# Kernel tuning notes

Measured on AMD Instinct MI355X. Metric: run time of the kernel, lower is better.

The kernel has to match this reference:

```python
import jax, jax.numpy as jnp
import numpy as np

BLOCK_SIZES = [256] * 8            # sum = N_CTX = 2048
B, H, D = 2, 16, 64
N_CTX = sum(BLOCK_SIZES)
SPARSITY_PATTERN = 'block_causal'  # row_starts = 0, row_ends = end of own block


def _build_masks(block_sizes, pattern):
    cs = np.cumsum([0] + list(block_sizes))
    row_ends = np.concatenate([np.full(bs, cs[i + 1], dtype=np.int32)
                               for i, bs in enumerate(block_sizes)])
    if pattern == 'block_diagonal':
        row_starts = np.concatenate([np.full(bs, cs[i], dtype=np.int32)
                                     for i, bs in enumerate(block_sizes)])
    elif pattern == 'block_causal':
        row_starts = np.zeros_like(row_ends)
    else:
        raise ValueError(pattern)
    return jnp.asarray(row_starts), jnp.asarray(row_ends)


def setup_inputs() -> dict:
    key = jax.random.key(0)
    kq, kk, kv = jax.random.split(key, 3)
    q = jax.random.normal(kq, (B, H, N_CTX, D), dtype=jnp.float32)
    k = jax.random.normal(kk, (B, H, N_CTX, D), dtype=jnp.float32)
    v = jax.random.normal(kv, (B, H, N_CTX, D), dtype=jnp.float32)
    row_starts, row_ends = _build_masks(BLOCK_SIZES, SPARSITY_PATTERN)
    sm_scale = jnp.float32(1.0 / np.sqrt(D))
    return {"q": q, "k": k, "v": v, "sm_scale": sm_scale,
            "row_starts": row_starts, "row_ends": row_ends}


def reference(q, k, v, sm_scale, row_starts, row_ends):
    # q,k,v: [B,H,N,D]; per query row i, attend to kv cols in [row_starts[i], row_ends[i])
    n = q.shape[2]
    cols = jnp.arange(n, dtype=jnp.int32)
    allowed = (cols[None, :] >= row_starts[:, None]) & (cols[None, :] < row_ends[:, None])  # [N,N]
    scores = jnp.einsum('bhqd,bhkd->bhqk', q, k) * sm_scale
    neg = jnp.finfo(scores.dtype).min
    scores = jnp.where(allowed[None, None], scores, neg)
    p = jax.nn.softmax(scores, axis=-1)
    return jnp.einsum('bhqk,bhkd->bhqd', p, v)
```

## Files before the change

kernel.cpp:

```cpp
#include <hip/hip_runtime.h>


typedef short bf16x8 __attribute__((ext_vector_type(8)));
typedef float f32x4  __attribute__((ext_vector_type(4)));
typedef unsigned short u16;
typedef u16 u16x8 __attribute__((ext_vector_type(8)));

#define MFMA(A,B,C) __builtin_amdgcn_mfma_f32_16x16x32_bf16((A),(B),(C),0,0,0)

__device__ __forceinline__ u16 f2bf_rne(float f) {
    union { float f; unsigned u; } c; c.f = f;
    unsigned r = c.u + 0x7FFFu + ((c.u >> 16) & 1u);
    return (u16)(r >> 16);
}
__device__ __forceinline__ u16 f2bf_fast(float f) {
    union { float f; unsigned u; } c; c.f = f;
    return (u16)((c.u + 0x8000u) >> 16);
}

__device__ __forceinline__ void gload_lds16(const void* g, void* lds) {
    __builtin_amdgcn_global_load_lds(
        (const __attribute__((address_space(1))) unsigned int*)g,
        (__attribute__((address_space(3))) unsigned int*)lds, 16, 0, 0);
}

__global__ __launch_bounds__(256)
void prep_kernel(const float* __restrict__ K, const float* __restrict__ V,
                 u16* __restrict__ blob)
{
    int bt = blockIdx.x;
    int tid = threadIdx.x;
    const size_t gbase = (size_t)bt * 4096;
    u16* bb = blob + (size_t)bt * 8192;
    __shared__ __align__(16) u16 lt[4096];
    {
        int key = tid >> 2, c2 = (tid & 3) << 1;
        int rotb = (key & 3) + 4 * ((key >> 3) & 1);
        const float* kp = K + gbase + key * 64 + c2 * 8;
        float4 x0 = *(const float4*)kp,       x1 = *(const float4*)(kp + 4);
        float4 x2 = *(const float4*)(kp + 8), x3 = *(const float4*)(kp + 12);
        u16x8 a, b;
        a[0]=f2bf_rne(x0.x); a[1]=f2bf_rne(x0.y); a[2]=f2bf_rne(x0.z); a[3]=f2bf_rne(x0.w);
        a[4]=f2bf_rne(x1.x); a[5]=f2bf_rne(x1.y); a[6]=f2bf_rne(x1.z); a[7]=f2bf_rne(x1.w);
        b[0]=f2bf_rne(x2.x); b[1]=f2bf_rne(x2.y); b[2]=f2bf_rne(x2.z); b[3]=f2bf_rne(x2.w);
        b[4]=f2bf_rne(x3.x); b[5]=f2bf_rne(x3.y); b[6]=f2bf_rne(x3.z); b[7]=f2bf_rne(x3.w);
        *(u16x8*)&bb[key * 64 + (((c2    ) + rotb) & 7) * 8] = a;
        *(u16x8*)&bb[key * 64 + (((c2 + 1) + rotb) & 7) * 8] = b;
    }
    {
        int wv = tid >> 6, ln = tid & 63;
        const float* vp = V + gbase + ln * 64 + wv * 16;
        float4 y0 = *(const float4*)vp,       y1 = *(const float4*)(vp + 4);
        float4 y2 = *(const float4*)(vp + 8), y3 = *(const float4*)(vp + 12);
        float yy[16] = { y0.x,y0.y,y0.z,y0.w, y1.x,y1.y,y1.z,y1.w,
                         y2.x,y2.y,y2.z,y2.w, y3.x,y3.y,y3.z,y3.w };
        int kc = ln >> 3, kw = ln & 7;
        #pragma unroll
        for (int j = 0; j < 16; ++j) {
            int d = wv * 16 + j;
            lt[d * 64 + ((kc + (j & 7)) & 7) * 8 + kw] = f2bf_rne(yy[j]);
        }
    }
    __syncthreads();
    {
        int o = tid * 16;
        *(u16x8*)&bb[4096 + o]     = *(const u16x8*)&lt[o];
        *(u16x8*)&bb[4096 + o + 8] = *(const u16x8*)&lt[o + 8];
    }
}

__global__ __launch_bounds__(256, 4)
void bsattn_main(const float* __restrict__ Q, const float* __restrict__ SC,
                 const int* __restrict__ RS, const int* __restrict__ RE,
                 const u16* __restrict__ blob, float* __restrict__ O)
{
    constexpr int N = 2048, D = 64;
    int wg = blockIdx.x;
    int bh = wg & 31;
    int i0 = wg >> 5, kk = i0 & 7, rr = i0 >> 3;
    int qt = (rr == 0) ? ((kk < 4) ? 28 + kk : 20 + kk)
           : (rr == 1) ? ((kk < 4) ? 20 + kk : 12 + kk)
           : (rr == 2) ? (8 + kk) : kk;
    int q0 = qt << 6;

    int tid = threadIdx.x, wid = tid >> 6, lane = tid & 63;
    int n = lane & 15, g = lane >> 4;

    __shared__ __align__(16) u16 lsm[16384];
    __shared__ int sbi[16];

    int myrow = q0 + wid * 16 + n;
    int rs_l = RS[myrow], re_l = RE[myrow];
    int w_rs_min = rs_l, w_rs_max = rs_l, w_re_min = re_l, w_re_max = re_l;
    #pragma unroll
    for (int o = 1; o < 16; o <<= 1) {
        w_rs_min = min(w_rs_min, __shfl_xor(w_rs_min, o));
        w_rs_max = max(w_rs_max, __shfl_xor(w_rs_max, o));
        w_re_min = min(w_re_min, __shfl_xor(w_re_min, o));
        w_re_max = max(w_re_max, __shfl_xor(w_re_max, o));
    }
    if (lane == 0) { sbi[wid * 2] = w_rs_min; sbi[wid * 2 + 1] = w_re_max; }

    float sscale = SC[0] * 1.44269504088896340736f;

    bf16x8 qf0, qf1;
    {
        const float* qp = Q + ((size_t)bh * N + myrow) * D + g * 8;
        float4 a0 = *(const float4*)qp,        a1 = *(const float4*)(qp + 4);
        float4 b0 = *(const float4*)(qp + 32), b1 = *(const float4*)(qp + 36);
        qf0[0]=f2bf_rne(a0.x*sscale); qf0[1]=f2bf_rne(a0.y*sscale);
        qf0[2]=f2bf_rne(a0.z*sscale); qf0[3]=f2bf_rne(a0.w*sscale);
        qf0[4]=f2bf_rne(a1.x*sscale); qf0[5]=f2bf_rne(a1.y*sscale);
        qf0[6]=f2bf_rne(a1.z*sscale); qf0[7]=f2bf_rne(a1.w*sscale);
        qf1[0]=f2bf_rne(b0.x*sscale); qf1[1]=f2bf_rne(b0.y*sscale);
        qf1[2]=f2bf_rne(b0.z*sscale); qf1[3]=f2bf_rne(b0.w*sscale);
        qf1[4]=f2bf_rne(b1.x*sscale); qf1[5]=f2bf_rne(b1.y*sscale);
        qf1[6]=f2bf_rne(b1.z*sscale); qf1[7]=f2bf_rne(b1.w*sscale);
    }

    __syncthreads();
    int kst  = min(min(sbi[0], sbi[2]), min(sbi[4], sbi[6])) & ~63;
    int kend = max(max(sbi[1], sbi[3]), max(sbi[5], sbi[7]));
    int t0 = kst >> 6;
    int w  = (kend - kst + 63) >> 6;

    int rA   = ((n >> 2) << 3) + (n & 3);
    int phk  = (n & 3) + 4 * ((n >> 2) & 1);
    int osA0 = rA * 64 + ((g + phk) & 7) * 8;
    int osA1 = rA * 64 + ((g + 4 + phk) & 7) * 8;
    int ov0  = 4096 + n * 64 + ((    g + (n & 7)) & 7) * 8;
    int ov1  = 4096 + n * 64 + ((4 + g + (n & 7)) & 7) * 8;

    f32x4 acc[4], accl = {0.f, 0.f, 0.f, 0.f};
    #pragma unroll
    for (int c = 0; c < 4; ++c) acc[c] = (f32x4){0.f, 0.f, 0.f, 0.f};
    bf16x8 ones;
    #pragma unroll
    for (int j = 0; j < 8; ++j) ones[j] = (short)0x3F80;

    auto stage = [&](int i) {
        if (i < w) {
            const u16* src = blob + (size_t)(bh * 32 + t0 + i) * 8192;
            u16* dst = &lsm[(i & 1) << 13];
            int wb = wid * 2048;
            #pragma unroll
            for (int c = 0; c < 4; ++c)
                gload_lds16(src + wb + c * 512 + lane * 8, dst + wb + c * 512);
        }
    };

    auto proc = [&](int kb, const u16* ls) {
        float sc[16];
        #pragma unroll
        for (int h = 0; h < 2; ++h) {
            int hb = h * 2048;
            f32x4 t0v = {0.f,0.f,0.f,0.f}, t1v = t0v;
            t0v = MFMA(*(const bf16x8*)&ls[hb + osA0],       qf0, t0v);
            t0v = MFMA(*(const bf16x8*)&ls[hb + osA1],       qf1, t0v);
            t1v = MFMA(*(const bf16x8*)&ls[hb + osA0 + 256], qf0, t1v);
            t1v = MFMA(*(const bf16x8*)&ls[hb + osA1 + 256], qf1, t1v);
            #pragma unroll
            for (int r = 0; r < 4; ++r) { sc[h*8 + r] = t0v[r]; sc[h*8 + 4 + r] = t1v[r]; }
        }
        if (kb < w_rs_max || kb + 64 > w_re_min) {
            #pragma unroll
            for (int h = 0; h < 2; ++h)
                #pragma unroll
                for (int j = 0; j < 8; ++j) {
                    int key = kb + h * 32 + g * 8 + j;
                    if (key < rs_l || key >= re_l) sc[h*8 + j] = -1e30f;
                }
        }
        bf16x8 pf0, pf1;
        #pragma unroll
        for (int j = 0; j < 8; ++j) { float p = __builtin_amdgcn_exp2f(sc[j]);     pf0[j] = (short)f2bf_fast(p); }
        #pragma unroll
        for (int j = 0; j < 8; ++j) { float p = __builtin_amdgcn_exp2f(sc[8 + j]); pf1[j] = (short)f2bf_fast(p); }
        #pragma unroll
        for (int h = 0; h < 2; ++h) {
            const bf16x8& pf = h ? pf1 : pf0;
            int ov = h ? ov1 : ov0;
            acc[0] = MFMA(pf, *(const bf16x8*)&ls[ov       ], acc[0]);
            acc[1] = MFMA(pf, *(const bf16x8*)&ls[ov + 1024], acc[1]);
            acc[2] = MFMA(pf, *(const bf16x8*)&ls[ov + 2048], acc[2]);
            acc[3] = MFMA(pf, *(const bf16x8*)&ls[ov + 3072], acc[3]);
            accl   = MFMA(pf, ones, accl);
        }
    };

    stage(0);
    for (int i = 0; i < w; ++i) {
        __syncthreads();
        stage(i + 1);
        proc(kst + (i << 6), &lsm[(i & 1) << 13]);
    }

    int rb = g << 2;
    int orow = q0 + wid * 16 + rb;
    float* ob = O + ((size_t)bh * N + orow) * D + n;
    #pragma unroll
    for (int r = 0; r < 4; ++r) {
        float li = 1.0f / accl[r];
        float* rp = ob + (size_t)r * D;
        rp[0]  = acc[0][r] * li;
        rp[16] = acc[1][r] * li;
        rp[32] = acc[2][r] * li;
        rp[48] = acc[3][r] * li;
    }
}

extern "C" void kernel_launch(void* const* d_in, const int* in_sizes, int n_in,
                              void* d_out, int out_size, void* d_ws, size_t ws_size,
                              hipStream_t stream) {
    const float* q  = (const float*)d_in[0];
    const float* k  = (const float*)d_in[1];
    const float* v  = (const float*)d_in[2];
    const float* sc = (const float*)d_in[3];
    const int* rs   = (const int*)d_in[4];
    const int* re   = (const int*)d_in[5];
    float* out      = (float*)d_out;
    u16* blob       = (u16*)d_ws;

    prep_kernel<<<dim3(1024), dim3(256), 0, stream>>>(k, v, blob);
    bsattn_main<<<dim3(1024), dim3(256), 0, stream>>>(q, sc, rs, re, blob, out);
}
```

Baseline: 131.4 us.

## Switch to single-wave 32x32x16 MFMA tiles with barrier-free double buffering

Rewrites the attention kernel so each workgroup is one 64-lane wave handling 32 query rows. It uses 32x32x16 bf16 MFMAs instead of 16x16x32, with new K/V LDS swizzles to match, set in the prep kernel. Workgroup barriers are replaced by vmcnt waits, and the wave prefetches two tiles ahead. Each wave now stages the full 16 KB K/V tile into LDS by itself, so global-to-LDS traffic grows per query row and occupancy depends on LDS per 64-thread block.

```diff
diff --git a/kernel.cpp b/kernel.cpp
--- a/kernel.cpp
+++ b/kernel.cpp
@@ -2,11 +2,11 @@
 
 
 typedef short bf16x8 __attribute__((ext_vector_type(8)));
-typedef float f32x4  __attribute__((ext_vector_type(4)));
+typedef float f32x16 __attribute__((ext_vector_type(16)));
 typedef unsigned short u16;
 typedef u16 u16x8 __attribute__((ext_vector_type(8)));
 
-#define MFMA(A,B,C) __builtin_amdgcn_mfma_f32_16x16x32_bf16((A),(B),(C),0,0,0)
+#define MFMA32(A,B,C) __builtin_amdgcn_mfma_f32_32x32x16_bf16((A),(B),(C),0,0,0)
 
 __device__ __forceinline__ u16 f2bf_rne(float f) {
     union { float f; unsigned u; } c; c.f = f;
@@ -17,7 +17,6 @@
     union { float f; unsigned u; } c; c.f = f;
     return (u16)((c.u + 0x8000u) >> 16);
 }
-
 __device__ __forceinline__ void gload_lds16(const void* g, void* lds) {
     __builtin_amdgcn_global_load_lds(
         (const __attribute__((address_space(1))) unsigned int*)g,
@@ -33,9 +32,11 @@
     const size_t gbase = (size_t)bt * 4096;
     u16* bb = blob + (size_t)bt * 8192;
     __shared__ __align__(16) u16 lt[4096];
-    {
-        int key = tid >> 2, c2 = (tid & 3) << 1;
-        int rotb = (key & 3) + 4 * ((key >> 3) & 1);
+
+    int key = tid >> 2;
+    int dg  = tid & 3;
+    {
+        int c2 = dg << 1;
         const float* kp = K + gbase + key * 64 + c2 * 8;
         float4 x0 = *(const float4*)kp,       x1 = *(const float4*)(kp + 4);
         float4 x2 = *(const float4*)(kp + 8), x3 = *(const float4*)(kp + 12);
@@ -44,21 +45,22 @@
         a[4]=f2bf_rne(x1.x); a[5]=f2bf_rne(x1.y); a[6]=f2bf_rne(x1.z); a[7]=f2bf_rne(x1.w);
         b[0]=f2bf_rne(x2.x); b[1]=f2bf_rne(x2.y); b[2]=f2bf_rne(x2.z); b[3]=f2bf_rne(x2.w);
         b[4]=f2bf_rne(x3.x); b[5]=f2bf_rne(x3.y); b[6]=f2bf_rne(x3.z); b[7]=f2bf_rne(x3.w);
-        *(u16x8*)&bb[key * 64 + (((c2    ) + rotb) & 7) * 8] = a;
-        *(u16x8*)&bb[key * 64 + (((c2 + 1) + rotb) & 7) * 8] = b;
-    }
-    {
-        int wv = tid >> 6, ln = tid & 63;
-        const float* vp = V + gbase + ln * 64 + wv * 16;
+        *(u16x8*)&bb[key * 64 + (((c2    ) + key) & 7) * 8] = a;
+        *(u16x8*)&bb[key * 64 + (((c2 + 1) + key) & 7) * 8] = b;
+    }
+    {
+        int sl = (key & 51) | ((key & 4) << 1) | ((key & 8) >> 1);
+        int sh = sl >> 3, sw = sl & 7;
+        const float* vp = V + gbase + key * 64 + dg * 16;
         float4 y0 = *(const float4*)vp,       y1 = *(const float4*)(vp + 4);
         float4 y2 = *(const float4*)(vp + 8), y3 = *(const float4*)(vp + 12);
         float yy[16] = { y0.x,y0.y,y0.z,y0.w, y1.x,y1.y,y1.z,y1.w,
                          y2.x,y2.y,y2.z,y2.w, y3.x,y3.y,y3.z,y3.w };
-        int kc = ln >> 3, kw = ln & 7;
         #pragma unroll
         for (int j = 0; j < 16; ++j) {
-            int d = wv * 16 + j;
-            lt[d * 64 + ((kc + (j & 7)) & 7) * 8 + kw] = f2bf_rne(yy[j]);
+            int d = dg * 16 + j;
+            int p = (sh + (j & 7) + 2 * dg) & 7;
+            lt[d * 64 + p * 8 + sw] = f2bf_rne(yy[j]);
         }
     }
     __syncthreads();
@@ -69,7 +71,7 @@
     }
 }
 
-__global__ __launch_bounds__(256, 4)
+__global__ __launch_bounds__(64)
 void bsattn_main(const float* __restrict__ Q, const float* __restrict__ SC,
                  const int* __restrict__ RS, const int* __restrict__ RE,
                  const u16* __restrict__ blob, float* __restrict__ O)
@@ -77,135 +79,122 @@
     constexpr int N = 2048, D = 64;
     int wg = blockIdx.x;
     int bh = wg & 31;
-    int i0 = wg >> 5, kk = i0 & 7, rr = i0 >> 3;
-    int qt = (rr == 0) ? ((kk < 4) ? 28 + kk : 20 + kk)
-           : (rr == 1) ? ((kk < 4) ? 20 + kk : 12 + kk)
-           : (rr == 2) ? (8 + kk) : kk;
-    int q0 = qt << 6;
-
-    int tid = threadIdx.x, wid = tid >> 6, lane = tid & 63;
-    int n = lane & 15, g = lane >> 4;
+    int qs = 63 - (wg >> 5);
+    int q0w = qs << 5;
+    int lane = threadIdx.x;
+    int n5 = lane & 31, h5 = lane >> 5;
 
     __shared__ __align__(16) u16 lsm[16384];
-    __shared__ int sbi[16];
-
-    int myrow = q0 + wid * 16 + n;
+
+    int myrow = q0w + n5;
     int rs_l = RS[myrow], re_l = RE[myrow];
     int w_rs_min = rs_l, w_rs_max = rs_l, w_re_min = re_l, w_re_max = re_l;
     #pragma unroll
-    for (int o = 1; o < 16; o <<= 1) {
+    for (int o = 1; o < 32; o <<= 1) {
         w_rs_min = min(w_rs_min, __shfl_xor(w_rs_min, o));
         w_rs_max = max(w_rs_max, __shfl_xor(w_rs_max, o));
         w_re_min = min(w_re_min, __shfl_xor(w_re_min, o));
         w_re_max = max(w_re_max, __shfl_xor(w_re_max, o));
     }
-    if (lane == 0) { sbi[wid * 2] = w_rs_min; sbi[wid * 2 + 1] = w_re_max; }
 
     float sscale = SC[0] * 1.44269504088896340736f;
 
-    bf16x8 qf0, qf1;
-    {
-        const float* qp = Q + ((size_t)bh * N + myrow) * D + g * 8;
-        float4 a0 = *(const float4*)qp,        a1 = *(const float4*)(qp + 4);
-        float4 b0 = *(const float4*)(qp + 32), b1 = *(const float4*)(qp + 36);
-        qf0[0]=f2bf_rne(a0.x*sscale); qf0[1]=f2bf_rne(a0.y*sscale);
-        qf0[2]=f2bf_rne(a0.z*sscale); qf0[3]=f2bf_rne(a0.w*sscale);
-        qf0[4]=f2bf_rne(a1.x*sscale); qf0[5]=f2bf_rne(a1.y*sscale);
-        qf0[6]=f2bf_rne(a1.z*sscale); qf0[7]=f2bf_rne(a1.w*sscale);
-        qf1[0]=f2bf_rne(b0.x*sscale); qf1[1]=f2bf_rne(b0.y*sscale);
-        qf1[2]=f2bf_rne(b0.z*sscale); qf1[3]=f2bf_rne(b0.w*sscale);
-        qf1[4]=f2bf_rne(b1.x*sscale); qf1[5]=f2bf_rne(b1.y*sscale);
-        qf1[6]=f2bf_rne(b1.z*sscale); qf1[7]=f2bf_rne(b1.w*sscale);
-    }
-
-    __syncthreads();
-    int kst  = min(min(sbi[0], sbi[2]), min(sbi[4], sbi[6])) & ~63;
-    int kend = max(max(sbi[1], sbi[3]), max(sbi[5], sbi[7]));
-    int t0 = kst >> 6;
-    int w  = (kend - kst + 63) >> 6;
-
-    int rA   = ((n >> 2) << 3) + (n & 3);
-    int phk  = (n & 3) + 4 * ((n >> 2) & 1);
-    int osA0 = rA * 64 + ((g + phk) & 7) * 8;
-    int osA1 = rA * 64 + ((g + 4 + phk) & 7) * 8;
-    int ov0  = 4096 + n * 64 + ((    g + (n & 7)) & 7) * 8;
-    int ov1  = 4096 + n * 64 + ((4 + g + (n & 7)) & 7) * 8;
-
-    f32x4 acc[4], accl = {0.f, 0.f, 0.f, 0.f};
-    #pragma unroll
-    for (int c = 0; c < 4; ++c) acc[c] = (f32x4){0.f, 0.f, 0.f, 0.f};
+    bf16x8 qf[4];
+    {
+        const float* qp = Q + ((size_t)bh * N + myrow) * D + h5 * 8;
+        #pragma unroll
+        for (int s = 0; s < 4; ++s) {
+            float4 x0 = *(const float4*)(qp + 16 * s);
+            float4 x1 = *(const float4*)(qp + 16 * s + 4);
+            qf[s][0] = f2bf_rne(x0.x * sscale); qf[s][1] = f2bf_rne(x0.y * sscale);
+            qf[s][2] = f2bf_rne(x0.z * sscale); qf[s][3] = f2bf_rne(x0.w * sscale);
+            qf[s][4] = f2bf_rne(x1.x * sscale); qf[s][5] = f2bf_rne(x1.y * sscale);
+            qf[s][6] = f2bf_rne(x1.z * sscale); qf[s][7] = f2bf_rne(x1.w * sscale);
+        }
+    }
+
+    int kst = w_rs_min & ~63;
+    int w   = (w_re_max - kst + 63) >> 6;
+
+    int rot = (h5 + (n5 & 7)) & 7;
+    int offK[2][4], offV[2][4];
+    #pragma unroll
+    for (int s = 0; s < 4; ++s) {
+        offK[0][s] = n5 * 64        + (((2*s + rot)) & 7) * 8;
+        offK[1][s] = (32 + n5) * 64 + (((2*s + rot)) & 7) * 8;
+        int v0t = 2 * ((n5 >> 4) & 3);
+        int v1t = 2 * ((2 + (n5 >> 4)) & 3);
+        offV[0][s] = 4096 + n5 * 64        + ((2*s + rot + v0t) & 7) * 8;
+        offV[1][s] = 4096 + (32 + n5) * 64 + ((2*s + rot + v1t) & 7) * 8;
+    }
+
+    f32x16 acc0, acc1, accl;
+    #pragma unroll
+    for (int r = 0; r < 16; ++r) { acc0[r] = 0.f; acc1[r] = 0.f; accl[r] = 0.f; }
     bf16x8 ones;
     #pragma unroll
     for (int j = 0; j < 8; ++j) ones[j] = (short)0x3F80;
 
     auto stage = [&](int i) {
         if (i < w) {
-            const u16* src = blob + (size_t)(bh * 32 + t0 + i) * 8192;
+            const u16* src = blob + ((size_t)(bh * 32) + (kst >> 6) + i) * 8192;
             u16* dst = &lsm[(i & 1) << 13];
-            int wb = wid * 2048;
             #pragma unroll
-            for (int c = 0; c < 4; ++c)
-                gload_lds16(src + wb + c * 512 + lane * 8, dst + wb + c * 512);
+            for (int cc = 0; cc < 16; ++cc)
+                gload_lds16(src + cc * 512 + lane * 8, dst + cc * 512);
         }
     };
 
     auto proc = [&](int kb, const u16* ls) {
-        float sc[16];
-        #pragma unroll
-        for (int h = 0; h < 2; ++h) {
-            int hb = h * 2048;
-            f32x4 t0v = {0.f,0.f,0.f,0.f}, t1v = t0v;
-            t0v = MFMA(*(const bf16x8*)&ls[hb + osA0],       qf0, t0v);
-            t0v = MFMA(*(const bf16x8*)&ls[hb + osA1],       qf1, t0v);
-            t1v = MFMA(*(const bf16x8*)&ls[hb + osA0 + 256], qf0, t1v);
-            t1v = MFMA(*(const bf16x8*)&ls[hb + osA1 + 256], qf1, t1v);
-            #pragma unroll
-            for (int r = 0; r < 4; ++r) { sc[h*8 + r] = t0v[r]; sc[h*8 + 4 + r] = t1v[r]; }
+        f32x16 c0, c1;
+        #pragma unroll
+        for (int r = 0; r < 16; ++r) { c0[r] = 0.f; c1[r] = 0.f; }
+        #pragma unroll
+        for (int s = 0; s < 4; ++s) {
+            c0 = MFMA32(*(const bf16x8*)&ls[offK[0][s]], qf[s], c0);
+            c1 = MFMA32(*(const bf16x8*)&ls[offK[1][s]], qf[s], c1);
         }
         if (kb < w_rs_max || kb + 64 > w_re_min) {
             #pragma unroll
-            for (int h = 0; h < 2; ++h)
-                #pragma unroll
-                for (int j = 0; j < 8; ++j) {
-                    int key = kb + h * 32 + g * 8 + j;
-                    if (key < rs_l || key >= re_l) sc[h*8 + j] = -1e30f;
-                }
-        }
-        bf16x8 pf0, pf1;
-        #pragma unroll
-        for (int j = 0; j < 8; ++j) { float p = __builtin_amdgcn_exp2f(sc[j]);     pf0[j] = (short)f2bf_fast(p); }
-        #pragma unroll
-        for (int j = 0; j < 8; ++j) { float p = __builtin_amdgcn_exp2f(sc[8 + j]); pf1[j] = (short)f2bf_fast(p); }
-        #pragma unroll
-        for (int h = 0; h < 2; ++h) {
-            const bf16x8& pf = h ? pf1 : pf0;
-            int ov = h ? ov1 : ov0;
-            acc[0] = MFMA(pf, *(const bf16x8*)&ls[ov       ], acc[0]);
-            acc[1] = MFMA(pf, *(const bf16x8*)&ls[ov + 1024], acc[1]);
-            acc[2] = MFMA(pf, *(const bf16x8*)&ls[ov + 2048], acc[2]);
-            acc[3] = MFMA(pf, *(const bf16x8*)&ls[ov + 3072], acc[3]);
-            accl   = MFMA(pf, ones, accl);
+            for (int r = 0; r < 16; ++r) {
+                int key = kb + (r & 3) + 8 * (r >> 2) + 4 * h5;
+                if (key < rs_l || key >= re_l)      c0[r] = -1e30f;
+                if (key + 32 < rs_l || key + 32 >= re_l) c1[r] = -1e30f;
+            }
+        }
+        bf16x8 pf[4];
+        #pragma unroll
+        for (int j = 0; j < 8; ++j) {
+            pf[0][j] = (short)f2bf_fast(__builtin_amdgcn_exp2f(c0[j]));
+            pf[1][j] = (short)f2bf_fast(__builtin_amdgcn_exp2f(c0[8 + j]));
+            pf[2][j] = (short)f2bf_fast(__builtin_amdgcn_exp2f(c1[j]));
+            pf[3][j] = (short)f2bf_fast(__builtin_amdgcn_exp2f(c1[8 + j]));
+        }
+        #pragma unroll
+        for (int s = 0; s < 4; ++s) {
+            acc0 = MFMA32(pf[s], *(const bf16x8*)&ls[offV[0][s]], acc0);
+            acc1 = MFMA32(pf[s], *(const bf16x8*)&ls[offV[1][s]], acc1);
+            accl = MFMA32(pf[s], ones, accl);
         }
     };
 
     stage(0);
+    stage(1);
     for (int i = 0; i < w; ++i) {
-        __syncthreads();
-        stage(i + 1);
+        if (i + 1 < w) __builtin_amdgcn_s_waitcnt(0x7FF0);
+        else           __builtin_amdgcn_s_waitcnt(0x3FF0);
+        __builtin_amdgcn_sched_barrier(0);
         proc(kst + (i << 6), &lsm[(i & 1) << 13]);
-    }
-
-    int rb = g << 2;
-    int orow = q0 + wid * 16 + rb;
-    float* ob = O + ((size_t)bh * N + orow) * D + n;
-    #pragma unroll
-    for (int r = 0; r < 4; ++r) {
+        stage(i + 2);
+    }
+
+    #pragma unroll
+    for (int r = 0; r < 16; ++r) {
+        int row = (r & 3) + 8 * (r >> 2) + 4 * h5;
         float li = 1.0f / accl[r];
-        float* rp = ob + (size_t)r * D;
-        rp[0]  = acc[0][r] * li;
-        rp[16] = acc[1][r] * li;
-        rp[32] = acc[2][r] * li;
-        rp[48] = acc[3][r] * li;
+        float* rp = O + ((size_t)bh * N + q0w + row) * D + n5;
+        rp[0]  = acc0[r] * li;
+        rp[32] = acc1[r] * li;
     }
 }
 
@@ -222,5 +211,5 @@
     u16* blob       = (u16*)d_ws;
 
     prep_kernel<<<dim3(1024), dim3(256), 0, stream>>>(k, v, blob);
-    bsattn_main<<<dim3(1024), dim3(256), 0, stream>>>(q, sc, rs, re, blob, out);
-}
+    bsattn_main<<<dim3(2048), dim3(64), 0, stream>>>(q, sc, rs, re, blob, out);
+}
```

After: 152.6 us. 16.2% more time.
